# Optimization experiments

Hardware: AMD Instinct MI355X
Metric: run time of the kernel (lower is better)

Reference implementation:

```python
import jax, jax.numpy as jnp
import numpy as np

B, S, D_IN, D_OUT = 4, 4096, 2048, 2048


def setup_inputs() -> dict:
    key = jax.random.key(0)
    kx, kw = jax.random.split(key)
    x = jax.random.normal(kx, (B, S, D_IN), dtype=jnp.float32)
    weight = jax.random.normal(kw, (D_OUT, D_IN), dtype=jnp.float32) * 0.02
    return {"x": x, "weight": weight}


def reference(x, weight):
    # Per-row absmax int8 activation quantization
    x_scale = jnp.clip(jnp.max(jnp.abs(x), axis=-1, keepdims=True), 1e-05, None)  # [B,S,1]
    x_quant = jnp.clip(jnp.round(x / x_scale * 127.0), -128.0, 127.0)
    # Ternary weight quantization (mean-centered absmean scale)
    w_mean = jnp.mean(weight)
    w_centered = weight - w_mean
    w_scale = jnp.clip(jnp.mean(jnp.abs(w_centered)), 1e-05, None)
    w_quant = jnp.clip(jnp.round(w_centered / w_scale), -1.0, 1.0)
    # GEMM on quantized values, then dequant rescale
    y = jnp.einsum('bsi,oi->bso', x_quant, w_quant)  # [B,S,D_OUT]
    y = y * (w_scale * x_scale / 127.0)
    return y.astype(x.dtype)
```

## Files before the change

kernel.cpp:

```cpp
#include <hip/hip_runtime.h>
#include <stdint.h>

#define M_TOT 16384
#define K_DIM 2048
#define N_DIM 2048
#define W_ELEMS (N_DIM * K_DIM)

typedef int v4i __attribute__((ext_vector_type(4)));

__device__ __forceinline__ void async_load16(const void* gptr, void* lptr) {
    __builtin_amdgcn_global_load_lds(
        (__attribute__((address_space(1))) void*)(uintptr_t)gptr,
        (__attribute__((address_space(3))) void*)(uint32_t)(uintptr_t)lptr,
        16, 0, 0);
}

__global__ void wsum_kernel(const float* __restrict__ w, double* __restrict__ sums) {
    int tid = blockIdx.x * 256 + threadIdx.x;
    const float4* w4 = (const float4*)w;
    double s = 0.0;
    for (int i = tid; i < W_ELEMS / 4; i += 512 * 256) {
        float4 v = w4[i];
        s += (double)v.x + (double)v.y + (double)v.z + (double)v.w;
    }
    #pragma unroll
    for (int off = 32; off; off >>= 1) s += __shfl_down(s, off);
    __shared__ double ls[4];
    if ((threadIdx.x & 63) == 0) ls[threadIdx.x >> 6] = s;
    __syncthreads();
    if (threadIdx.x == 0) atomicAdd(&sums[0], ls[0] + ls[1] + ls[2] + ls[3]);
}

__global__ void wabs_kernel(const float* __restrict__ w, double* __restrict__ sums) {
    double mean = sums[0] * (1.0 / (double)W_ELEMS);
    int tid = blockIdx.x * 256 + threadIdx.x;
    const float4* w4 = (const float4*)w;
    double s = 0.0;
    for (int i = tid; i < W_ELEMS / 4; i += 512 * 256) {
        float4 v = w4[i];
        s += fabs((double)v.x - mean) + fabs((double)v.y - mean) +
             fabs((double)v.z - mean) + fabs((double)v.w - mean);
    }
    #pragma unroll
    for (int off = 32; off; off >>= 1) s += __shfl_down(s, off);
    __shared__ double ls[4];
    if ((threadIdx.x & 63) == 0) ls[threadIdx.x >> 6] = s;
    __syncthreads();
    if (threadIdx.x == 0) atomicAdd(&sums[1], ls[0] + ls[1] + ls[2] + ls[3]);
}

__device__ __forceinline__ int qclamp(float v, int lo, int hi) {
    int q = (int)rintf(v);
    q = q > hi ? hi : (q < lo ? lo : q);
    return q & 255;
}

__global__ void wquant_kernel(const float* __restrict__ w, const double* __restrict__ sums,
                              int8_t* __restrict__ wq) {
    float mean  = (float)(sums[0] * (1.0 / (double)W_ELEMS));
    float scale = (float)fmax(sums[1] * (1.0 / (double)W_ELEMS), 1e-5);
    int i = blockIdx.x * 256 + threadIdx.x;
    float4 v = ((const float4*)w)[i];
    int p = qclamp((v.x - mean) / scale, -1, 1)
          | (qclamp((v.y - mean) / scale, -1, 1) << 8)
          | (qclamp((v.z - mean) / scale, -1, 1) << 16)
          | (qclamp((v.w - mean) / scale, -1, 1) << 24);
    ((int*)wq)[i] = p;
}

__global__ void xquant_kernel(const float* __restrict__ x, int8_t* __restrict__ xq,
                              float* __restrict__ xscale) {
    int row = blockIdx.x;
    int t = threadIdx.x;
    const float4* xr = (const float4*)(x + (size_t)row * K_DIM);
    float4 v0 = xr[t];
    float4 v1 = xr[t + 256];
    float m = fmaxf(fmaxf(fmaxf(fabsf(v0.x), fabsf(v0.y)), fmaxf(fabsf(v0.z), fabsf(v0.w))),
                    fmaxf(fmaxf(fabsf(v1.x), fabsf(v1.y)), fmaxf(fabsf(v1.z), fabsf(v1.w))));
    #pragma unroll
    for (int off = 32; off; off >>= 1) m = fmaxf(m, __shfl_down(m, off));
    __shared__ float ls[4];
    if ((t & 63) == 0) ls[t >> 6] = m;
    __syncthreads();
    float scale = fmaxf(fmaxf(fmaxf(ls[0], ls[1]), fmaxf(ls[2], ls[3])), 1e-5f);
    if (t == 0) xscale[row] = scale;
    int* outp = (int*)(xq + (size_t)row * K_DIM);
    int p0 = qclamp(v0.x / scale * 127.0f, -128, 127)
           | (qclamp(v0.y / scale * 127.0f, -128, 127) << 8)
           | (qclamp(v0.z / scale * 127.0f, -128, 127) << 16)
           | (qclamp(v0.w / scale * 127.0f, -128, 127) << 24);
    int p1 = qclamp(v1.x / scale * 127.0f, -128, 127)
           | (qclamp(v1.y / scale * 127.0f, -128, 127) << 8)
           | (qclamp(v1.z / scale * 127.0f, -128, 127) << 16)
           | (qclamp(v1.w / scale * 127.0f, -128, 127) << 24);
    outp[t]       = p0;
    outp[t + 256] = p1;
}

__global__ __launch_bounds__(256) void gemm_i8_kernel(
    const int8_t* __restrict__ xq, const int8_t* __restrict__ wq,
    const float* __restrict__ xscale, const double* __restrict__ sums,
    float* __restrict__ out)
{
    __shared__ __align__(16) int8_t lsA[128 * 64];
    __shared__ __align__(16) int8_t lsB[128 * 64];
    const int tid  = threadIdx.x;
    const int lane = tid & 63;
    const int wv   = tid >> 6;
    const int bm = blockIdx.y, bn = blockIdx.x;

    const int8_t* gA = xq + (size_t)bm * 128 * K_DIM;
    const int8_t* gB = wq + (size_t)bn * 128 * K_DIM;

    const int r = tid >> 2;
    const int s = tid & 3;
    const int c = s ^ ((r >> 1) & 3);
    const size_t gOff0 = (size_t)r * K_DIM + c * 16;
    const size_t gOff1 = gOff0 + (size_t)64 * K_DIM;

    v4i acc[4][4] = {};

    const int wm = (wv >> 1) * 64;
    const int wn = (wv & 1) * 64;
    const int fc = lane >> 4;
    const int fr = lane & 15;

    int aoff[4], boff[4];
    #pragma unroll
    for (int i = 0; i < 4; i++) {
        int ra = wm + i * 16 + fr;
        aoff[i] = ra * 64 + (fc ^ ((ra >> 1) & 3)) * 16;
        int rb = wn + i * 16 + fr;
        boff[i] = rb * 64 + (fc ^ ((rb >> 1) & 3)) * 16;
    }

    for (int k0 = 0; k0 < K_DIM; k0 += 64) {
        __syncthreads();
        async_load16(gA + gOff0 + k0, lsA + tid * 16);
        async_load16(gA + gOff1 + k0, lsA + 4096 + tid * 16);
        async_load16(gB + gOff0 + k0, lsB + tid * 16);
        async_load16(gB + gOff1 + k0, lsB + 4096 + tid * 16);
        __syncthreads();

        v4i af[4], bf[4];
        #pragma unroll
        for (int i = 0; i < 4; i++) af[i] = *(const v4i*)(lsA + aoff[i]);
        #pragma unroll
        for (int i = 0; i < 4; i++) bf[i] = *(const v4i*)(lsB + boff[i]);

        #pragma unroll
        for (int mi = 0; mi < 4; mi++)
            #pragma unroll
            for (int nj = 0; nj < 4; nj++)
                acc[mi][nj] = __builtin_amdgcn_mfma_i32_16x16x64_i8(
                    af[mi], bf[nj], acc[mi][nj], 0, 0, 0);
    }

    float wscale = (float)fmax(sums[1] * (1.0 / (double)W_ELEMS), 1e-5);
    float f127 = wscale * (1.0f / 127.0f);
    #pragma unroll
    for (int mi = 0; mi < 4; mi++) {
        #pragma unroll
        for (int rg = 0; rg < 4; rg++) {
            int mg = bm * 128 + wm + mi * 16 + (lane >> 4) * 4 + rg;
            float fs = f127 * xscale[mg];
            float* orow = out + (size_t)mg * N_DIM + bn * 128 + wn;
            #pragma unroll
            for (int nj = 0; nj < 4; nj++)
                orow[nj * 16 + fr] = fs * (float)acc[mi][nj][rg];
        }
    }
}

extern "C" void kernel_launch(void* const* d_in, const int* in_sizes, int n_in,
                              void* d_out, int out_size, void* d_ws, size_t ws_size,
                              hipStream_t stream) {
    const float* x = (const float*)d_in[0];
    const float* w = (const float*)d_in[1];
    float* out = (float*)d_out;

    char* ws = (char*)d_ws;
    double* sums   = (double*)ws;
    float*  xscale = (float*)(ws + 64);
    int8_t* xq     = (int8_t*)(ws + 64 + 65536);
    int8_t* wq     = (int8_t*)(ws + 64 + 65536 + (size_t)M_TOT * K_DIM);

    hipMemsetAsync(sums, 0, 16, stream);
    wsum_kernel <<<512, 256, 0, stream>>>(w, sums);
    wabs_kernel <<<512, 256, 0, stream>>>(w, sums);
    wquant_kernel<<<W_ELEMS / 1024, 256, 0, stream>>>(w, sums, wq);
    xquant_kernel<<<M_TOT, 256, 0, stream>>>(x, xq, xscale);
    gemm_i8_kernel<<<dim3(N_DIM / 128, M_TOT / 128), 256, 0, stream>>>(xq, wq, xscale, sums, out);
}
```

Before: 338.4 us.

## Widen GEMM block tile to 128x256 and use reciprocal scale in xquant

The int8 GEMM block tile grows from 128x128 to 128x256 along N. Each wave now computes a 64x128 sub-tile with 32 accumulator fragments, which raises the number of MFMAs per A fragment loaded and halves the number of times A tiles are reloaded. This costs more accumulator registers, which can lower occupancy, and the grid shrinks to 8x128 blocks. Separately, x quantization multiplies by a precomputed reciprocal instead of dividing per element, which may change rounding slightly at ties.

```diff
diff --git a/kernel.cpp b/kernel.cpp
--- a/kernel.cpp
+++ b/kernel.cpp
@@ -85,14 +85,15 @@
     float scale = fmaxf(fmaxf(fmaxf(ls[0], ls[1]), fmaxf(ls[2], ls[3])), 1e-5f);
     if (t == 0) xscale[row] = scale;
     int* outp = (int*)(xq + (size_t)row * K_DIM);
-    int p0 = qclamp(v0.x / scale * 127.0f, -128, 127)
-           | (qclamp(v0.y / scale * 127.0f, -128, 127) << 8)
-           | (qclamp(v0.z / scale * 127.0f, -128, 127) << 16)
-           | (qclamp(v0.w / scale * 127.0f, -128, 127) << 24);
-    int p1 = qclamp(v1.x / scale * 127.0f, -128, 127)
-           | (qclamp(v1.y / scale * 127.0f, -128, 127) << 8)
-           | (qclamp(v1.z / scale * 127.0f, -128, 127) << 16)
-           | (qclamp(v1.w / scale * 127.0f, -128, 127) << 24);
+    float inv = 127.0f / scale;
+    int p0 = qclamp(v0.x * inv, -128, 127)
+           | (qclamp(v0.y * inv, -128, 127) << 8)
+           | (qclamp(v0.z * inv, -128, 127) << 16)
+           | (qclamp(v0.w * inv, -128, 127) << 24);
+    int p1 = qclamp(v1.x * inv, -128, 127)
+           | (qclamp(v1.y * inv, -128, 127) << 8)
+           | (qclamp(v1.z * inv, -128, 127) << 16)
+           | (qclamp(v1.w * inv, -128, 127) << 24);
     outp[t]       = p0;
     outp[t + 256] = p1;
 }
@@ -103,55 +104,59 @@
     float* __restrict__ out)
 {
     __shared__ __align__(16) int8_t lsA[128 * 64];
-    __shared__ __align__(16) int8_t lsB[128 * 64];
+    __shared__ __align__(16) int8_t lsB[256 * 64];
     const int tid  = threadIdx.x;
     const int lane = tid & 63;
     const int wv   = tid >> 6;
-    const int bm = blockIdx.y, bn = blockIdx.x;
+    const int bn = blockIdx.x, bm = blockIdx.y;
 
     const int8_t* gA = xq + (size_t)bm * 128 * K_DIM;
-    const int8_t* gB = wq + (size_t)bn * 128 * K_DIM;
+    const int8_t* gB = wq + (size_t)bn * 256 * K_DIM;
 
     const int r = tid >> 2;
     const int s = tid & 3;
     const int c = s ^ ((r >> 1) & 3);
     const size_t gOff0 = (size_t)r * K_DIM + c * 16;
-    const size_t gOff1 = gOff0 + (size_t)64 * K_DIM;
 
-    v4i acc[4][4] = {};
+    v4i acc[4][8] = {};
 
     const int wm = (wv >> 1) * 64;
-    const int wn = (wv & 1) * 64;
+    const int wn = (wv & 1) * 128;
     const int fc = lane >> 4;
     const int fr = lane & 15;
 
-    int aoff[4], boff[4];
+    int aoff[4], boff[8];
     #pragma unroll
     for (int i = 0; i < 4; i++) {
         int ra = wm + i * 16 + fr;
         aoff[i] = ra * 64 + (fc ^ ((ra >> 1) & 3)) * 16;
-        int rb = wn + i * 16 + fr;
-        boff[i] = rb * 64 + (fc ^ ((rb >> 1) & 3)) * 16;
+    }
+    #pragma unroll
+    for (int j = 0; j < 8; j++) {
+        int rb = wn + j * 16 + fr;
+        boff[j] = rb * 64 + (fc ^ ((rb >> 1) & 3)) * 16;
     }
 
     for (int k0 = 0; k0 < K_DIM; k0 += 64) {
         __syncthreads();
-        async_load16(gA + gOff0 + k0, lsA + tid * 16);
-        async_load16(gA + gOff1 + k0, lsA + 4096 + tid * 16);
-        async_load16(gB + gOff0 + k0, lsB + tid * 16);
-        async_load16(gB + gOff1 + k0, lsB + 4096 + tid * 16);
+        async_load16(gA + gOff0 + k0,                          lsA + tid * 16);
+        async_load16(gA + gOff0 + (size_t) 64 * K_DIM + k0,    lsA + 4096  + tid * 16);
+        async_load16(gB + gOff0 + k0,                          lsB + tid * 16);
+        async_load16(gB + gOff0 + (size_t) 64 * K_DIM + k0,    lsB + 4096  + tid * 16);
+        async_load16(gB + gOff0 + (size_t)128 * K_DIM + k0,    lsB + 8192  + tid * 16);
+        async_load16(gB + gOff0 + (size_t)192 * K_DIM + k0,    lsB + 12288 + tid * 16);
         __syncthreads();
 
-        v4i af[4], bf[4];
+        v4i af[4], bf[8];
         #pragma unroll
         for (int i = 0; i < 4; i++) af[i] = *(const v4i*)(lsA + aoff[i]);
         #pragma unroll
-        for (int i = 0; i < 4; i++) bf[i] = *(const v4i*)(lsB + boff[i]);
+        for (int j = 0; j < 8; j++) bf[j] = *(const v4i*)(lsB + boff[j]);
 
         #pragma unroll
         for (int mi = 0; mi < 4; mi++)
             #pragma unroll
-            for (int nj = 0; nj < 4; nj++)
+            for (int nj = 0; nj < 8; nj++)
                 acc[mi][nj] = __builtin_amdgcn_mfma_i32_16x16x64_i8(
                     af[mi], bf[nj], acc[mi][nj], 0, 0, 0);
     }
@@ -164,9 +169,9 @@
         for (int rg = 0; rg < 4; rg++) {
             int mg = bm * 128 + wm + mi * 16 + (lane >> 4) * 4 + rg;
             float fs = f127 * xscale[mg];
-            float* orow = out + (size_t)mg * N_DIM + bn * 128 + wn;
+            float* orow = out + (size_t)mg * N_DIM + bn * 256 + wn;
             #pragma unroll
-            for (int nj = 0; nj < 4; nj++)
+            for (int nj = 0; nj < 8; nj++)
                 orow[nj * 16 + fr] = fs * (float)acc[mi][nj][rg];
         }
     }
@@ -190,5 +195,5 @@
     wabs_kernel <<<512, 256, 0, stream>>>(w, sums);
     wquant_kernel<<<W_ELEMS / 1024, 256, 0, stream>>>(w, sums, wq);
     xquant_kernel<<<M_TOT, 256, 0, stream>>>(x, xq, xscale);
-    gemm_i8_kernel<<<dim3(N_DIM / 128, M_TOT / 128), 256, 0, stream>>>(xq, wq, xscale, sums, out);
+    gemm_i8_kernel<<<dim3(N_DIM / 256, M_TOT / 128), 256, 0, stream>>>(xq, wq, xscale, sums, out);
 }
```

Result: slower. 390.5 us (+15.4%).
